# Kernel tuning notes

Hardware: AMD Instinct MI355X
Metric: run time of the kernel (lower is better)

The kernel has to match this reference:

```python
import jax, jax.numpy as jnp
import numpy as np

B, S, D, H = 2, 2048, 1024, 16
DK = D // H


def setup_inputs() -> dict:
    key = jax.random.key(0)
    ks = jax.random.split(key, 13)
    scale = 1.0 / np.sqrt(D)
    return {
        "query": jax.random.normal(ks[0], (B, S, D), jnp.float32),
        "key": jax.random.normal(ks[1], (B, S, D), jnp.float32),
        "value": jax.random.normal(ks[2], (B, S, D), jnp.float32),
        "mask": jax.random.randint(ks[3], (B, S, S), 0, 2, jnp.int32),
        "Wq": jax.random.normal(ks[4], (D, D), jnp.float32) * scale,
        "bq": jnp.zeros((D,), jnp.float32),
        "Wk": jax.random.normal(ks[5], (D, D), jnp.float32) * scale,
        "bk": jnp.zeros((D,), jnp.float32),
        "Wv": jax.random.normal(ks[6], (D, D), jnp.float32) * scale,
        "bv": jnp.zeros((D,), jnp.float32),
        "Wo": jax.random.normal(ks[7], (D, D), jnp.float32) * scale,
        "bo": jnp.zeros((D,), jnp.float32),
    }


def _split_heads(x):
    # [B,S,D] -> [B,H,S,DK]
    b, s, _ = x.shape
    return x.reshape(b, s, H, DK).transpose(0, 2, 1, 3)


def reference(query, key, value, mask, Wq, bq, Wk, bk, Wv, bv, Wo, bo):
    q = _split_heads(query @ Wq + bq)
    k = _split_heads(key @ Wk + bk)
    v = _split_heads(value @ Wv + bv)
    # scaled dot-product scores [B,H,Sq,Sk]
    scores = jnp.einsum("bhqd,bhkd->bhqk", q, k) / jnp.sqrt(jnp.float32(DK))
    scores = jnp.where(mask[:, None, :, :] == 0, jnp.float32(-1e9), scores)
    p_attn = jax.nn.softmax(scores, axis=-1)  # dropout p=0.0 -> identity
    x = jnp.einsum("bhqk,bhkd->bhqd", p_attn, v)
    x = x.transpose(0, 2, 1, 3).reshape(query.shape[0], -1, D)
    return x @ Wo + bo
```

## Files before the change

### kernel.cpp

```cpp
#include <hip/hip_runtime.h>
#include <cstdint>

#define B_ 2
#define S_ 2048
#define D_ 1024
#define H_ 16
#define DK_ 64
#define SCALE_ 0.18033688011112042f

typedef float f32x4 __attribute__((ext_vector_type(4)));
typedef float f32x16 __attribute__((ext_vector_type(16)));
typedef __bf16 bf16x8 __attribute__((ext_vector_type(8)));
typedef unsigned short u16x8 __attribute__((ext_vector_type(8)));
typedef unsigned short u16x4 __attribute__((ext_vector_type(4)));
typedef unsigned int u32x4 __attribute__((ext_vector_type(4)));

__device__ __forceinline__ unsigned short f2bf(float x) {
  unsigned int u = __builtin_bit_cast(unsigned int, x);
  u += 0x7FFFu + ((u >> 16) & 1u);
  return (unsigned short)(u >> 16);
}

__device__ __forceinline__ void gload16(const void* g, void* l) {
  __builtin_amdgcn_global_load_lds((__attribute__((address_space(1))) void*)(void*)g,
                                   (__attribute__((address_space(3))) void*)l, 16, 0, 0);
}

__device__ __forceinline__ float exp2v(float x) {
  float r;
  asm("v_exp_f32 %0, %1" : "=v"(r) : "v"(x));
  return r;
}

__device__ __forceinline__ unsigned int cvtpk(float a, float b) {
  unsigned int r;
  asm("v_cvt_pk_bf16_f32 %0, %1, %2" : "=v"(r) : "v"(a), "v"(b));
  return r;
}

__device__ __forceinline__ unsigned int bit_mask(unsigned int w, int bit) {
#if __has_builtin(__builtin_amdgcn_sbfe)
  return (unsigned int)__builtin_amdgcn_sbfe((int)w, bit, 1);
#else
  return (unsigned int)((int)(w << (31 - bit)) >> 31);
#endif
}

__global__ __launch_bounds__(256) void prep_kernel(
    const float* __restrict__ w0, const float* __restrict__ w1,
    const float* __restrict__ w2, const float* __restrict__ w3,
    unsigned short* o0, unsigned short* o1, unsigned short* o2, unsigned short* o3,
    const int* __restrict__ mask, unsigned int* __restrict__ mb) {
  __shared__ float t[32][33];
  const int bid = blockIdx.x;
  const int tid = threadIdx.x;
  if (bid < 4096) {
    const int z = bid >> 10, rr = bid & 1023;
    const float* W;
    unsigned short* O;
    float sc = 1.f;
    if (z == 0) { W = w0; O = o0; sc = SCALE_; }
    else if (z == 1) { W = w1; O = o1; }
    else if (z == 2) { W = w2; O = o2; }
    else { W = w3; O = o3; }
    const int n0 = (rr & 31) * 32, k0 = (rr >> 5) * 32;
    const int tx = tid & 31, ty = tid >> 5;
    for (int i = ty; i < 32; i += 8) t[i][tx] = W[(size_t)(k0 + i) * D_ + n0 + tx];
    __syncthreads();
    for (int i = ty; i < 32; i += 8) O[(size_t)(n0 + i) * D_ + k0 + tx] = f2bf(t[tx][i] * sc);
  } else {
    const int wid = ((bid - 4096) << 2) + (tid >> 6);
    const int lane = tid & 63;
    size_t base = (size_t)wid << 6;
    unsigned long long bits = __ballot(mask[base + lane] != 0);
    if (lane == 0) *(unsigned long long*)(mb + (base >> 5)) = bits;
  }
}

template <int MODE, int TM, int TN, int NWM, int NWN, bool AF32>
__device__ __forceinline__ void gemm_t(const void* __restrict__ Ap,
                                       const unsigned short* __restrict__ BT,
                                       const float* __restrict__ bias, float bsc,
                                       void* __restrict__ Cp,
                                       unsigned short* __restrict__ AlS,
                                       unsigned short* __restrict__ BlS,
                                       int M, int N, int K) {
  static_assert(NWM * NWN == 4, "4 waves");
  constexpr int WM = TM / NWM;
  constexpr int WN = TN / NWN;
  constexpr int MR = WM / 16, NR = WN / 16;
  constexpr int ASTRIDE = TM * 32;
  constexpr int BSTRIDE = TN * 32;
  const unsigned short* A16 = (const unsigned short*)Ap;
  const float* A32 = (const float*)Ap;
  const int tid = threadIdx.x;
  const int lane = tid & 63;
  const int w = tid >> 6;
  const int wr = w / NWN, wc = w % NWN;
  const int nwg = gridDim.x * gridDim.y;
  const int wg = blockIdx.x + gridDim.x * blockIdx.y;
  const int work = (wg & 7) * (nwg >> 3) + (wg >> 3);
  const int nx = N / TN;
  const int m0 = (work / nx) * TM, n0 = (work % nx) * TN;

  f32x4 acc[MR][NR] = {};
  const int nk = K / 32;
  const int srow = lane >> 2;
  const int sxor = ((lane & 3) ^ ((srow >> 1) & 3)) * 8;
  const int scol_lin = (lane & 3) * 8;

  const int fr = lane & 15;
  const int rsw = ((lane >> 4) ^ ((fr >> 1) & 3)) * 8;

  auto stageB = [&](int kt, int bufi) {
#pragma unroll
    for (int it = 0; it < TN / 64; ++it) {
      int chunk = it * 4 + w;
      gload16(BT + (size_t)(n0 + chunk * 16 + srow) * K + kt * 32 + sxor,
              BlS + bufi * BSTRIDE + chunk * 512);
    }
  };
  auto stageA16 = [&](int kt, int bufi) {
#pragma unroll
    for (int it = 0; it < TM / 64; ++it) {
      int chunk = it * 4 + w;
      gload16(A16 + (size_t)(m0 + chunk * 16 + srow) * K + kt * 32 + sxor,
              AlS + bufi * ASTRIDE + chunk * 512);
    }
  };

  auto loadA32 = [&](int kt, f32x4 (&aR)[TM / 64][2]) {
#pragma unroll
    for (int it = 0; it < TM / 64; ++it) {
      int chunk = it * 4 + w;
      const float* ga = A32 + (size_t)(m0 + chunk * 16 + srow) * K + kt * 32 + scol_lin;
      aR[it][0] = *(const f32x4*)ga;
      aR[it][1] = *(const f32x4*)(ga + 4);
    }
  };
  auto writeA = [&](int bufi, f32x4 (&aR)[TM / 64][2]) {
#pragma unroll
    for (int it = 0; it < TM / 64; ++it) {
      int chunk = it * 4 + w;
      u32x4 pk;
      pk[0] = cvtpk(aR[it][0][0], aR[it][0][1]);
      pk[1] = cvtpk(aR[it][0][2], aR[it][0][3]);
      pk[2] = cvtpk(aR[it][1][0], aR[it][1][1]);
      pk[3] = cvtpk(aR[it][1][2], aR[it][1][3]);
      *(u32x4*)(AlS + bufi * ASTRIDE + chunk * 512 + srow * 32 + sxor) = pk;
    }
  };
  auto compute = [&](int bufi) {
    bf16x8 af[MR], bf[NR];
#pragma unroll
    for (int i = 0; i < MR; ++i)
      af[i] = __builtin_bit_cast(bf16x8,
          *(const u16x8*)(AlS + bufi * ASTRIDE + (wr * WM + i * 16 + fr) * 32 + rsw));
#pragma unroll
    for (int j = 0; j < NR; ++j)
      bf[j] = __builtin_bit_cast(bf16x8,
          *(const u16x8*)(BlS + bufi * BSTRIDE + (wc * WN + j * 16 + fr) * 32 + rsw));
    __builtin_amdgcn_s_setprio(1);
#pragma unroll
    for (int i = 0; i < MR; ++i)
#pragma unroll
      for (int j = 0; j < NR; ++j)
        acc[i][j] = __builtin_amdgcn_mfma_f32_16x16x32_bf16(af[i], bf[j], acc[i][j], 0, 0, 0);
    __builtin_amdgcn_s_setprio(0);
  };

  if (AF32) {
    f32x4 a0[TM / 64][2], a1[TM / 64][2];
    loadA32(0, a0);
    writeA(0, a0);
    loadA32(1, a0);
    stageB(0, 0);
    for (int kt = 0; kt < nk; kt += 2) {
      __syncthreads();
      stageB(kt + 1, 1);
      if (kt + 2 < nk) loadA32(kt + 2, a1);
      compute(0);
      writeA(1, a0);
      __syncthreads();
      if (kt + 2 < nk) {
        stageB(kt + 2, 0);
        if (kt + 3 < nk) loadA32(kt + 3, a0);
        compute(1);
        writeA(0, a1);
      } else {
        compute(1);
      }
    }
  } else {
    stageA16(0, 0);
    stageB(0, 0);
    for (int kt = 0; kt < nk; ++kt) {
      const int buf = kt & 1;
      __syncthreads();
      if (kt + 1 < nk) {
        stageB(kt + 1, buf ^ 1);
        stageA16(kt + 1, buf ^ 1);
      }
      compute(buf);
    }
  }

  const int rg = (lane >> 4) * 4;
  const int cg = lane & 15;
#pragma unroll
  for (int i = 0; i < MR; ++i)
#pragma unroll
    for (int j = 0; j < NR; ++j) {
      int col = n0 + wc * WN + j * 16 + cg;
      float bv = bias[col] * bsc;
#pragma unroll
      for (int e = 0; e < 4; ++e) {
        int row = m0 + wr * WM + i * 16 + rg + e;
        float v = acc[i][j][e] + bv;
        if (MODE == 1)
          ((float*)Cp)[(size_t)row * N + col] = v;
        else if (MODE == 0)
          ((unsigned short*)Cp)[(size_t)row * N + col] = f2bf(v);
        else
          ((unsigned short*)Cp)[((size_t)(row >> 11) * D_ + col) * S_ + (row & (S_ - 1))] = f2bf(v);
      }
    }
}

__global__ __launch_bounds__(256) void qkv_gemm_kernel(
    const float* __restrict__ query, const float* __restrict__ key,
    const float* __restrict__ value, const unsigned short* __restrict__ wtq,
    const unsigned short* __restrict__ wtk, const unsigned short* __restrict__ wtv,
    const float* __restrict__ bq, const float* __restrict__ bk, const float* __restrict__ bv,
    unsigned short* q, unsigned short* k, unsigned short* vt) {
  __shared__ alignas(16) unsigned short As[2 * 64 * 32];
  __shared__ alignas(16) unsigned short Bs[2 * 128 * 32];
  if (blockIdx.z == 0)
    gemm_t<0, 64, 128, 2, 2, true>(query, wtq, bq, SCALE_, (void*)q, As, Bs, B_ * S_, D_, D_);
  else if (blockIdx.z == 1)
    gemm_t<0, 64, 128, 2, 2, true>(key, wtk, bk, 1.f, (void*)k, As, Bs, B_ * S_, D_, D_);
  else
    gemm_t<2, 64, 128, 2, 2, true>(value, wtv, bv, 1.f, (void*)vt, As, Bs, B_ * S_, D_, D_);
}

__global__ __launch_bounds__(256) void out_gemm_kernel(const unsigned short* __restrict__ x,
                                                       const unsigned short* __restrict__ wto,
                                                       const float* __restrict__ bo,
                                                       float* __restrict__ out) {
  __shared__ alignas(16) unsigned short As[2 * 128 * 32];
  __shared__ alignas(16) unsigned short Bs[2 * 64 * 32];
  gemm_t<1, 128, 64, 4, 1, false>(x, wto, bo, 1.f, (void*)out, As, Bs, B_ * S_, D_, D_);
}

__global__ __launch_bounds__(256, 2) void attn_kernel(const unsigned short* __restrict__ Q,
                                                      const unsigned short* __restrict__ K,
                                                      const unsigned short* __restrict__ Vt,
                                                      const unsigned int* __restrict__ mb,
                                                      unsigned short* __restrict__ X) {
  __shared__ unsigned short Kl[2][128 * 64];
  __shared__ unsigned short Vl[2][2][64 * 64];

  const int tid = threadIdx.x;
  const int lane = tid & 63;
  const int w = tid >> 6;
  const int ql = lane & 31;
  const int hi = lane >> 5;

  const int wg = blockIdx.x + gridDim.x * blockIdx.y;
  const int swz = (wg & 7) * 64 + (wg >> 3);
  const int qt = swz & 15;
  const int bh = swz >> 4;
  const int b = bh >> 4, h = bh & 15;
  const int q_g = qt * 128 + w * 32 + ql;

  const size_t qkbase = ((size_t)b * S_) * D_ + h * DK_;
  const size_t vtbase = ((size_t)b * D_ + h * DK_) * S_;

  bf16x8 qf[4];
  {
    const unsigned short* qp = Q + qkbase + (size_t)q_g * D_ + hi * 8;
#pragma unroll
    for (int c = 0; c < 4; ++c)
      qf[c] = __builtin_bit_cast(bf16x8, *(const u16x8*)(qp + c * 16));
  }

  const int lr = lane >> 3;
  const int seg = (lane & 7) ^ lr;
  const unsigned short* Ks = K + qkbase + (size_t)(w * 32 + lr) * D_ + seg * 8;
  const unsigned short* Vs = Vt + vtbase + (size_t)(w * 16 + lr) * S_ + seg * 8;

  auto stage = [&](int kt, int bufi) {
#pragma unroll
    for (int c = 0; c < 4; ++c)
      gload16(Ks + ((size_t)kt * 128 + c * 8) * D_, &Kl[bufi][(w * 32 + c * 8) * 64]);
#pragma unroll
    for (int c = 0; c < 4; ++c)
      gload16(Vs + (size_t)((c & 1) * 8) * S_ + kt * 128 + (c >> 1) * 64,
              &Vl[bufi][c >> 1][(w * 16 + (c & 1) * 8) * 64]);
  };

  const unsigned long long* mrow =
      (const unsigned long long*)mb + ((size_t)b * S_ + q_g) * 32;

  f32x16 o0 = {}, o1 = {};
  f32x16 o2 = {};
  const int sw = (ql & 7) << 4;

  const unsigned int one2 = 0x3F803F80u;
  const bf16x8 onesf = __builtin_bit_cast(bf16x8, u32x4{one2, one2, one2, one2});

  stage(0, 0);
  const int NT = S_ / 128;
  unsigned long long M0n = mrow[0], M1n = mrow[1];

  for (int kt = 0; kt < NT; ++kt) {
    const int buf = kt & 1;
    __syncthreads();
    unsigned long long M0 = M0n, M1 = M1n;

    bf16x8 kf[2][2][4];
#pragma unroll
    for (int hh = 0; hh < 2; ++hh) {
      const char* Kb = (const char*)&Kl[buf][hh * 64 * 64];
#pragma unroll
      for (int r = 0; r < 2; ++r)
#pragma unroll
        for (int c = 0; c < 4; ++c)
          kf[hh][r][c] = __builtin_bit_cast(
              bf16x8, *(const u16x8*)(Kb + (((r * 32 + ql) * 128 + c * 32 + hi * 16) ^ sw)));
    }
    if (kt < NT - 1) {
      stage(kt + 1, buf ^ 1);
      M0n = mrow[kt * 2 + 2];
      M1n = mrow[kt * 2 + 3];
    }

    f32x16 s[2][2] = {};
    __builtin_amdgcn_s_setprio(1);
#pragma unroll
    for (int hh = 0; hh < 2; ++hh)
#pragma unroll
      for (int c = 0; c < 4; ++c) {
        s[hh][0] = __builtin_amdgcn_mfma_f32_32x32x16_bf16(kf[hh][0][c], qf[c], s[hh][0], 0, 0, 0);
        s[hh][1] = __builtin_amdgcn_mfma_f32_32x32x16_bf16(kf[hh][1][c], qf[c], s[hh][1], 0, 0, 0);
      }
    __builtin_amdgcn_s_setprio(0);

    bf16x8 vf[2][2][4];
#pragma unroll
    for (int hh = 0; hh < 2; ++hh) {
      const char* Vb = (const char*)&Vl[buf][hh][0];
#pragma unroll
      for (int nt = 0; nt < 2; ++nt)
#pragma unroll
        for (int kc = 0; kc < 4; ++kc)
          vf[hh][nt][kc] = __builtin_bit_cast(
              bf16x8, *(const u16x8*)(Vb + (((nt * 32 + ql) * 128 + kc * 32 + hi * 16) ^ sw)));
    }

    u32x4 pw[2][4];
#pragma unroll
    for (int hh = 0; hh < 2; ++hh) {
      const unsigned long long M = hh ? M1 : M0;
      unsigned int W0 = (unsigned int)(M >> (hi * 4));
      unsigned int W1 = (unsigned int)(M >> (32 + hi * 4));
#pragma unroll
      for (int r = 0; r < 16; ++r) {
        const int krl = (r & 3) + 8 * (r >> 2);
        unsigned int mk0 = bit_mask(W0, krl);
        float p0 = exp2v(s[hh][0][r]);
        s[hh][0][r] = __builtin_bit_cast(float, __builtin_bit_cast(unsigned int, p0) & mk0);
        unsigned int mk1 = bit_mask(W1, krl);
        float p1 = exp2v(s[hh][1][r]);
        s[hh][1][r] = __builtin_bit_cast(float, __builtin_bit_cast(unsigned int, p1) & mk1);
      }
#pragma unroll
      for (int kc = 0; kc < 4; ++kc) {
        const int rb = (kc & 1) * 8;
        const int st = kc >> 1;
        unsigned int w0 = cvtpk(s[hh][st][rb + 0], s[hh][st][rb + 1]);
        unsigned int w1 = cvtpk(s[hh][st][rb + 2], s[hh][st][rb + 3]);
        unsigned int w2 = cvtpk(s[hh][st][rb + 4], s[hh][st][rb + 5]);
        unsigned int w3 = cvtpk(s[hh][st][rb + 6], s[hh][st][rb + 7]);
        unsigned int u0, u1, u2, u3;
#if __has_builtin(__builtin_amdgcn_permlane32_swap)
        { auto r02 = __builtin_amdgcn_permlane32_swap(w0, w2, false, false);
          u0 = r02[0]; u2 = r02[1]; }
        { auto r13 = __builtin_amdgcn_permlane32_swap(w1, w3, false, false);
          u1 = r13[0]; u3 = r13[1]; }
#else
        { unsigned int t0 = (unsigned int)__shfl_xor((int)w0, 32);
          unsigned int t2 = (unsigned int)__shfl_xor((int)w2, 32);
          u0 = hi ? t2 : w0; u2 = hi ? w2 : t0;
          unsigned int t1 = (unsigned int)__shfl_xor((int)w1, 32);
          unsigned int t3 = (unsigned int)__shfl_xor((int)w3, 32);
          u1 = hi ? t3 : w1; u3 = hi ? w3 : t1; }
#endif
        pw[hh][kc] = u32x4{u0, u1, u2, u3};
      }
    }

    __builtin_amdgcn_s_setprio(1);
#pragma unroll
    for (int hh = 0; hh < 2; ++hh)
#pragma unroll
      for (int kc = 0; kc < 4; ++kc) {
        bf16x8 pf = __builtin_bit_cast(bf16x8, pw[hh][kc]);
        o0 = __builtin_amdgcn_mfma_f32_32x32x16_bf16(vf[hh][0][kc], pf, o0, 0, 0, 0);
        o1 = __builtin_amdgcn_mfma_f32_32x32x16_bf16(vf[hh][1][kc], pf, o1, 0, 0, 0);
        o2 = __builtin_amdgcn_mfma_f32_32x32x16_bf16(onesf, pf, o2, 0, 0, 0);
      }
    __builtin_amdgcn_s_setprio(0);
  }

  float inv = 1.f / o2[0];
  unsigned short* Xp = X + ((size_t)b * S_ + q_g) * D_ + h * DK_;
#pragma unroll
  for (int rb = 0; rb < 4; ++rb) {
    int d0 = 8 * rb + 4 * hi;
    *(unsigned int*)(Xp + d0) = cvtpk(o0[4 * rb + 0] * inv, o0[4 * rb + 1] * inv);
    *(unsigned int*)(Xp + d0 + 2) = cvtpk(o0[4 * rb + 2] * inv, o0[4 * rb + 3] * inv);
    *(unsigned int*)(Xp + 32 + d0) = cvtpk(o1[4 * rb + 0] * inv, o1[4 * rb + 1] * inv);
    *(unsigned int*)(Xp + 32 + d0 + 2) = cvtpk(o1[4 * rb + 2] * inv, o1[4 * rb + 3] * inv);
  }
}

extern "C" void kernel_launch(void* const* d_in, const int* in_sizes, int n_in,
                              void* d_out, int out_size, void* d_ws, size_t ws_size,
                              hipStream_t stream) {
  const float* query = (const float*)d_in[0];
  const float* key = (const float*)d_in[1];
  const float* value = (const float*)d_in[2];
  const int* mask = (const int*)d_in[3];
  const float* Wq = (const float*)d_in[4];
  const float* bq = (const float*)d_in[5];
  const float* Wk = (const float*)d_in[6];
  const float* bk = (const float*)d_in[7];
  const float* Wv = (const float*)d_in[8];
  const float* bv = (const float*)d_in[9];
  const float* Wo = (const float*)d_in[10];
  const float* bo = (const float*)d_in[11];
  float* out = (float*)d_out;

  const size_t ACT = (size_t)B_ * S_ * D_;
  const size_t WSZ = (size_t)D_ * D_;
  unsigned short* ws = (unsigned short*)d_ws;
  unsigned short* wtq = ws;
  unsigned short* wtk = wtq + WSZ;
  unsigned short* wtv = wtk + WSZ;
  unsigned short* wto = wtv + WSZ;
  unsigned short* qb = wto + WSZ;
  unsigned short* kb = qb + ACT;
  unsigned short* vt = kb + ACT;
  unsigned int* mbp = (unsigned int*)(vt + ACT);
  unsigned short* xb = (unsigned short*)(mbp + (size_t)B_ * S_ * S_ / 32);

  prep_kernel<<<36864, 256, 0, stream>>>(Wq, Wk, Wv, Wo, wtq, wtk, wtv, wto, mask, mbp);

  dim3 gg(8, 64, 3);
  qkv_gemm_kernel<<<gg, 256, 0, stream>>>(query, key, value, wtq, wtk, wtv,
                                          bq, bk, bv, qb, kb, vt);

  dim3 ag(S_ / 128, B_ * H_);
  attn_kernel<<<ag, 256, 0, stream>>>(qb, kb, vt, mbp, xb);

  dim3 og(16, 32, 1);
  out_gemm_kernel<<<og, 256, 0, stream>>>(xb, wto, bo, out);
}
```

Before: 146.5 us.

## Restructure fp32-A GEMM pipeline with single register buffer and explicit waitcnt barriers

Replaces the two-register-buffer, two-step unrolled loop for fp32 A operands with a single-step loop that uses one register buffer. Each iteration stages B for the next tile, computes, writes the prefetched A tile to LDS, then issues the next A load. Synchronization uses explicit s_waitcnt with a partial vmcnt plus a raw s_barrier and sched_barrier instead of __syncthreads, so in-flight global loads need not fully drain. This is meant to lower register pressure and barrier stalls, but it depends on hand-counted vmcnt values being correct.

```diff
diff --git a/kernel.cpp b/kernel.cpp
--- a/kernel.cpp
+++ b/kernel.cpp
@@ -170,25 +170,27 @@
   };
 
   if (AF32) {
-    f32x4 a0[TM / 64][2], a1[TM / 64][2];
-    loadA32(0, a0);
-    writeA(0, a0);
-    loadA32(1, a0);
+    f32x4 aA[TM / 64][2];
+    loadA32(0, aA);
+    writeA(0, aA);
     stageB(0, 0);
-    for (int kt = 0; kt < nk; kt += 2) {
-      __syncthreads();
-      stageB(kt + 1, 1);
-      if (kt + 2 < nk) loadA32(kt + 2, a1);
-      compute(0);
-      writeA(1, a0);
-      __syncthreads();
-      if (kt + 2 < nk) {
-        stageB(kt + 2, 0);
-        if (kt + 3 < nk) loadA32(kt + 3, a0);
-        compute(1);
-        writeA(0, a1);
-      } else {
-        compute(1);
+    if (nk > 1) loadA32(1, aA);
+    asm volatile("s_waitcnt vmcnt(2) lgkmcnt(0)" ::: "memory");
+    __builtin_amdgcn_s_barrier();
+    __builtin_amdgcn_sched_barrier(0);
+    for (int kt = 0; kt < nk; ++kt) {
+      const int b = kt & 1;
+      if (kt + 1 < nk) stageB(kt + 1, b ^ 1);
+      compute(b);
+      if (kt + 1 < nk) writeA(b ^ 1, aA);
+      if (kt + 2 < nk) loadA32(kt + 2, aA);
+      if (kt + 1 < nk) {
+        if (kt + 2 < nk)
+          asm volatile("s_waitcnt vmcnt(2) lgkmcnt(0)" ::: "memory");
+        else
+          asm volatile("s_waitcnt vmcnt(0) lgkmcnt(0)" ::: "memory");
+        __builtin_amdgcn_s_barrier();
+        __builtin_amdgcn_sched_barrier(0);
       }
     }
   } else {
```

New measurement: 145.3 us (median of 2 runs). No clear change (-0.9%).
